# Kernel tuning notes

Measured on AMD Instinct MI355X. Metric: run time of the kernel, lower is better.

Reference implementation:

```python
import jax, jax.numpy as jnp
import numpy as np

K = 2           # top-k experts
TEMP = 1.0      # router temperature


def setup_inputs() -> dict:
    key = jax.random.key(0)
    k0, k1, k2, k3 = jax.random.split(key, 4)
    B, T, C, E = 4, 8192, 1024, 64
    x = jax.random.normal(k0, (B, T, C), dtype=jnp.float32)
    cond = jax.random.normal(k1, (B, C), dtype=jnp.float32)
    # nn.Linear weights: gate (E, C), cond_proj (C, 2C)
    Wg = jax.random.normal(k2, (E, C), dtype=jnp.float32) * 0.02
    Wc = jax.random.normal(k3, (C, 2 * C), dtype=jnp.float32) * 0.02
    return {"x": x, "cond": cond, "Wg": Wg, "Wc": Wc}


def reference(x, cond, Wg, Wc):
    B, T, C = x.shape
    E = Wg.shape[0]
    # conditioning path: broadcast cond over tokens, concat, project
    c_exp = jnp.broadcast_to(cond[:, None, :], (B, T, C))
    hc = jnp.concatenate([x, c_exp], axis=-1)          # (B,T,2C)
    h = jnp.einsum('btd,cd->btc', hc, Wc)              # (B,T,C)
    logits = jnp.einsum('btc,ec->bte', h, Wg) * (1.0 / TEMP)  # (B,T,E)
    probs = jax.nn.softmax(logits, axis=-1)
    topk_vals, idx = jax.lax.top_k(logits, K)          # (B,T,K), sorted desc
    scores = jax.nn.softmax(topk_vals, axis=-1)
    # aux stats (no_grad in torch)
    importance = jax.lax.stop_gradient(jnp.mean(probs, axis=(0, 1)))  # (E,)
    counts = jnp.zeros((E,), probs.dtype).at[idx.reshape(-1)].add(1.0)
    load = counts / jnp.clip(jnp.sum(counts), 1.0)
    load = jax.lax.stop_gradient(load)
    return (idx, scores, probs, importance, load)
```

## Files before the change

### kernel.cpp

```cpp
#include <hip/hip_runtime.h>
#include <math.h>

#define B_    4
#define T_    8192
#define C_    1024
#define E_    64
#define NTOK  (B_*T_)
#define KSEL  2

#define OFF_IDX    0
#define OFF_SCORES (NTOK*KSEL)
#define OFF_PROBS  (2*NTOK*KSEL)
#define OFF_IMP    (OFF_PROBS + NTOK*E_)
#define OFF_LOAD   (OFF_IMP + E_)

#define WS_W64    0
#define WS_W32    1048576
#define WS_BSWH   1310720
#define WS_BSWL   1441792
#define WS_LB64   1572864
#define WS_LB32   1574912
#define WS_CNT    1575936
#define WS_LIST   1576448

#define REFINE_CAP 8192
#define REFINE_EPS 3e-4f

typedef __attribute__((ext_vector_type(8))) short short8;
typedef __attribute__((ext_vector_type(4))) float f32x4;

__global__ __launch_bounds__(256) void k_comb(const float* __restrict__ Wg,
                                              const float* __restrict__ Wc,
                                              double* __restrict__ w64,
                                              float* __restrict__ out,
                                              unsigned int* __restrict__ ref_cnt) {
    __shared__ float wc_s[64 * 64];
    __shared__ float wg_s[64 * 64];
    const int tid   = threadIdx.x;
    const int e     = tid & 63;
    const int dg    = tid >> 6;
    const int dtile = (blockIdx.x & 31) * 64;
    const int cbase = (blockIdx.x >> 5) * 128;

    if (blockIdx.x == 0) {
        if (tid < 2 * E_) out[OFF_IMP + tid] = 0.f;
        if (tid == 2 * E_) *ref_cnt = 0u;
    }

    double acc[16];
#pragma unroll
    for (int i = 0; i < 16; ++i) acc[i] = 0.0;

    for (int cc = 0; cc < 128; cc += 64) {
        const int c0 = cbase + cc;
        __syncthreads();
#pragma unroll
        for (int k = 0; k < 4; ++k) {
            int li = tid + k * 256;
            int r = li >> 4, c4 = (li & 15) * 4;
            *(float4*)&wc_s[r * 64 + c4] =
                *(const float4*)&Wc[(size_t)(c0 + r) * 2048 + dtile + c4];
        }
#pragma unroll
        for (int k = 0; k < 4; ++k) {
            int li = tid + k * 256;
            int r = li >> 4, c4 = (li & 15) * 4;
            float4 v = *(const float4*)&Wg[(size_t)r * 1024 + c0 + c4];
            wg_s[(c4 + 0) * 64 + r] = v.x;
            wg_s[(c4 + 1) * 64 + r] = v.y;
            wg_s[(c4 + 2) * 64 + r] = v.z;
            wg_s[(c4 + 3) * 64 + r] = v.w;
        }
        __syncthreads();
        for (int c = 0; c < 64; ++c) {
            double wg = (double)wg_s[c * 64 + e];
            const float* wcrow = &wc_s[c * 64 + dg * 16];
#pragma unroll
            for (int i = 0; i < 16; ++i)
                acc[i] += wg * (double)wcrow[i];
        }
    }
#pragma unroll
    for (int i = 0; i < 16; ++i) {
        double* p = &w64[(size_t)(dtile + dg * 16 + i) * 64 + e];
#if __has_builtin(__builtin_amdgcn_global_atomic_fadd_f64)
        unsafeAtomicAdd(p, acc[i]);
#else
        atomicAdd(p, acc[i]);
#endif
    }
}

__global__ __launch_bounds__(256) void k_finalize(const double* __restrict__ w64,
                                                  const float* __restrict__ cond,
                                                  float* __restrict__ wcomb32,
                                                  short* __restrict__ bswH,
                                                  short* __restrict__ bswL,
                                                  double* __restrict__ lbias64,
                                                  float* __restrict__ lbias32) {
    const int tid = threadIdx.x;
    if (blockIdx.x < 64) {
        const int e  = blockIdx.x;
        const int et = e >> 4, nn = e & 15;
        for (int d = tid; d < 1024; d += 256) {
            float f = (float)w64[(size_t)d * 64 + e];
            wcomb32[d * 64 + e] = f;
            unsigned u = __float_as_uint(f);
            short hi = (short)(u >> 16);
            float r = f - __uint_as_float(u & 0xFFFF0000u);
            short lo = (short)(__float_as_uint(r) >> 16);
            int kchunk = d >> 5, qsel = (d >> 3) & 3, j = d & 7;
            int idx = ((kchunk * 4 + et) * 64 + qsel * 16 + nn) * 8 + j;
            bswH[idx] = hi;
            bswL[idx] = lo;
        }
    } else {
        const int b = blockIdx.x - 64;
        const int e = tid & 63, part = tid >> 6;
        double acc = 0.0;
        const int d0 = part * 256;
        for (int d = d0; d < d0 + 256; ++d)
            acc += (double)cond[b * 1024 + d] * w64[(size_t)(1024 + d) * 64 + e];
        __shared__ double red[256];
        red[tid] = acc;
        __syncthreads();
        if (tid < 64) {
            double s = red[tid] + red[tid + 64] + red[tid + 128] + red[tid + 192];
            lbias64[b * 64 + tid] = s;
            lbias32[b * 64 + tid] = (float)s;
        }
    }
}

__device__ __forceinline__ void cvt_split8(const float* __restrict__ p,
                                           short8& h, short8& l) {
    float4 v0 = *(const float4*)p;
    float4 v1 = *(const float4*)(p + 4);
    float xv[8] = {v0.x, v0.y, v0.z, v0.w, v1.x, v1.y, v1.z, v1.w};
#pragma unroll
    for (int j = 0; j < 8; ++j) {
        unsigned u = __float_as_uint(xv[j]);
        h[j] = (short)(u >> 16);
        float r = xv[j] - __uint_as_float(u & 0xFFFF0000u);
        l[j] = (short)(__float_as_uint(r) >> 16);
    }
}

#define MT    32
#define ROWP  65

__global__ __launch_bounds__(256, 4) void k_main(const float* __restrict__ x,
                                                 const short* __restrict__ bswH,
                                                 const short* __restrict__ bswL,
                                                 const float* __restrict__ lbias32,
                                                 float* __restrict__ out,
                                                 unsigned int* __restrict__ ref_cnt,
                                                 int* __restrict__ ref_list) {
    __shared__ float accbuf[4 * MT * ROWP];
    __shared__ float invs[MT];
    __shared__ unsigned int cnts[E_];

    const int tid    = threadIdx.x;
    const int wid    = tid >> 6;
    const int lane   = tid & 63;
    const int nn     = lane & 15;
    const int qsel   = lane >> 4;
    const int token0 = blockIdx.x * MT;
    const int b      = token0 >> 13;

    if (tid < E_) cnts[tid] = 0;

    f32x4 acc[2][4];
#pragma unroll
    for (int m = 0; m < 2; ++m)
#pragma unroll
        for (int et = 0; et < 4; ++et) acc[m][et] = (f32x4){0.f, 0.f, 0.f, 0.f};

    const float* a0 = x + (size_t)(token0 + nn) * 1024 + wid * 256 + qsel * 8;
    const float* a1 = a0 + (size_t)16 * 1024;
    const short* bh0 = bswH + ((size_t)(wid * 8) * 4) * 512 + lane * 8;
    const short* bl0 = bswL + ((size_t)(wid * 8) * 4) * 512 + lane * 8;

#pragma unroll 2
    for (int kc = 0; kc < 8; ++kc) {
        short8 ah0, al0, ah1, al1;
        cvt_split8(a0 + kc * 32, ah0, al0);
        cvt_split8(a1 + kc * 32, ah1, al1);
        const short* bh = bh0 + (size_t)kc * 4 * 512;
        const short* bl = bl0 + (size_t)kc * 4 * 512;
#pragma unroll
        for (int et = 0; et < 4; ++et) {
            short8 b_h = *(const short8*)(bh + et * 512);
            short8 b_l = *(const short8*)(bl + et * 512);
            acc[0][et] = __builtin_amdgcn_mfma_f32_16x16x32_bf16(ah0, b_h, acc[0][et], 0, 0, 0);
            acc[0][et] = __builtin_amdgcn_mfma_f32_16x16x32_bf16(ah0, b_l, acc[0][et], 0, 0, 0);
            acc[0][et] = __builtin_amdgcn_mfma_f32_16x16x32_bf16(al0, b_h, acc[0][et], 0, 0, 0);
            acc[1][et] = __builtin_amdgcn_mfma_f32_16x16x32_bf16(ah1, b_h, acc[1][et], 0, 0, 0);
            acc[1][et] = __builtin_amdgcn_mfma_f32_16x16x32_bf16(ah1, b_l, acc[1][et], 0, 0, 0);
            acc[1][et] = __builtin_amdgcn_mfma_f32_16x16x32_bf16(al1, b_h, acc[1][et], 0, 0, 0);
        }
    }

    const int q4 = qsel * 4;
#pragma unroll
    for (int m = 0; m < 2; ++m)
#pragma unroll
        for (int et = 0; et < 4; ++et)
#pragma unroll
            for (int r = 0; r < 4; ++r)
                accbuf[wid * (MT * ROWP) + (m * 16 + q4 + r) * ROWP + et * 16 + nn] =
                    acc[m][et][r];
    __syncthreads();

    for (int li = tid; li < MT * E_; li += 256) {
        int tok = li >> 6, e = li & 63;
        int o = tok * ROWP + e;
        float s = accbuf[o] + accbuf[MT * ROWP + o] + accbuf[2 * MT * ROWP + o] +
                  accbuf[3 * MT * ROWP + o] + lbias32[b * 64 + e];
        accbuf[o] = s;
    }
    __syncthreads();

    if (tid < MT) {
        const int t = tid;
        const int base = t * ROWP;
        float v1 = -1e30f, v2 = -1e30f, v3 = -1e30f;
        int i1 = 0, i2 = 0;
        for (int e = 0; e < E_; ++e) {
            float l = accbuf[base + e];
            if (l > v1)      { v3 = v2; v2 = v1; i2 = i1; v1 = l; i1 = e; }
            else if (l > v2) { v3 = v2; v2 = l; i2 = e; }
            else if (l > v3) { v3 = l; }
        }
        float sum = 0.f;
        for (int e = 0; e < E_; ++e) {
            float ex = __expf(accbuf[base + e] - v1);
            accbuf[base + e] = ex;
            sum += ex;
        }
        invs[t] = 1.0f / sum;

        const int gt = token0 + t;
        float s1 = 1.0f / (1.0f + __expf(v2 - v1));
        *(float2*)&out[OFF_IDX + (size_t)gt * 2]    = make_float2((float)i1, (float)i2);
        *(float2*)&out[OFF_SCORES + (size_t)gt * 2] = make_float2(s1, 1.0f - s1);
        atomicAdd(&cnts[i1], 1u);
        atomicAdd(&cnts[i2], 1u);

        float g12 = v1 - v2, g23 = v2 - v3;
        float g = g12 < g23 ? g12 : g23;
        if (g < REFINE_EPS) {
            unsigned int pos = atomicAdd(ref_cnt, 1u);
            if (pos < REFINE_CAP) ref_list[pos] = gt;
        }
    }
    __syncthreads();

    float* probs = out + OFF_PROBS + (size_t)token0 * E_;
#pragma unroll
    for (int k = 0; k < 2; ++k) {
        int li4 = tid + k * 256;
        int tok = li4 >> 4;
        int c4 = (li4 & 15) << 2;
        float inv = invs[tok];
        int o = tok * ROWP + c4;
        *(float4*)&probs[(size_t)li4 * 4] =
            make_float4(accbuf[o] * inv, accbuf[o + 1] * inv,
                        accbuf[o + 2] * inv, accbuf[o + 3] * inv);
    }

    if (tid < E_) {
        const int e = tid;
        float s = 0.f;
        for (int t = 0; t < MT; ++t) s += accbuf[t * ROWP + e] * invs[t];
        atomicAdd(&out[OFF_IMP + e],  s * (1.0f / (float)NTOK));
        atomicAdd(&out[OFF_LOAD + e], (float)cnts[e] * (1.0f / (float)(NTOK * KSEL)));
    }
}

__global__ __launch_bounds__(256) void k_refine(const float* __restrict__ x,
                                                const float* __restrict__ wcomb32,
                                                const double* __restrict__ lbias64,
                                                const unsigned int* __restrict__ ref_cnt,
                                                const int* __restrict__ ref_list,
                                                float* __restrict__ out) {
    int wave = (int)((blockIdx.x * blockDim.x + threadIdx.x) >> 6);
    int lane = threadIdx.x & 63;
    unsigned int n = *ref_cnt;
    if (n > REFINE_CAP) n = REFINE_CAP;
    const int nwaves = (int)((gridDim.x * blockDim.x) >> 6);

    for (unsigned int wi = wave; wi < n; wi += nwaves) {
        const int gt = ref_list[wi];
        const int b = gt / T_;
        const float* xrow = x + (size_t)gt * C_;
        double a0 = 0.0, a1 = 0.0, a2 = 0.0, a3 = 0.0;
        for (int d = 0; d < C_; d += 4) {
            a0 += (double)xrow[d + 0] * (double)wcomb32[(d + 0) * 64 + lane];
            a1 += (double)xrow[d + 1] * (double)wcomb32[(d + 1) * 64 + lane];
            a2 += (double)xrow[d + 2] * (double)wcomb32[(d + 2) * 64 + lane];
            a3 += (double)xrow[d + 3] * (double)wcomb32[(d + 3) * 64 + lane];
        }
        double acc = ((a0 + a1) + (a2 + a3)) + lbias64[b * 64 + lane];

        double v = acc; int id = lane;
        for (int off = 32; off > 0; off >>= 1) {
            double ov = __shfl_xor(v, off, 64);
            int oid   = __shfl_xor(id, off, 64);
            if (ov > v || (ov == v && oid < id)) { v = ov; id = oid; }
        }
        double v1 = v; int i1 = id;
        v = (lane == i1) ? -1e300 : acc; id = lane;
        for (int off = 32; off > 0; off >>= 1) {
            double ov = __shfl_xor(v, off, 64);
            int oid   = __shfl_xor(id, off, 64);
            if (ov > v || (ov == v && oid < id)) { v = ov; id = oid; }
        }
        double v2 = v; int i2 = id;

        if (lane == 0) {
            float s1 = (float)(1.0 / (1.0 + exp(v2 - v1)));
            *(float2*)&out[OFF_IDX + (size_t)gt * 2]    = make_float2((float)i1, (float)i2);
            *(float2*)&out[OFF_SCORES + (size_t)gt * 2] = make_float2(s1, 1.0f - s1);
        }
    }
}

extern "C" void kernel_launch(void* const* d_in, const int* in_sizes, int n_in,
                              void* d_out, int out_size, void* d_ws, size_t ws_size,
                              hipStream_t stream) {
    const float* x    = (const float*)d_in[0];
    const float* cond = (const float*)d_in[1];
    const float* Wg   = (const float*)d_in[2];
    const float* Wc   = (const float*)d_in[3];
    float* out = (float*)d_out;
    char*  ws  = (char*)d_ws;

    double* w64     = (double*)(ws + WS_W64);
    float*  wcomb32 = (float*)(ws + WS_W32);
    short*  bswH    = (short*)(ws + WS_BSWH);
    short*  bswL    = (short*)(ws + WS_BSWL);
    double* lbias64 = (double*)(ws + WS_LB64);
    float*  lbias32 = (float*)(ws + WS_LB32);
    unsigned int* ref_cnt = (unsigned int*)(ws + WS_CNT);
    int*    ref_list = (int*)(ws + WS_LIST);

    hipMemsetAsync(w64, 0, 2048 * 64 * sizeof(double), stream);

    k_comb<<<256, 256, 0, stream>>>(Wg, Wc, w64, out, ref_cnt);
    k_finalize<<<68, 256, 0, stream>>>(w64, cond, wcomb32, bswH, bswL, lbias64, lbias32);
    k_main<<<NTOK / MT, 256, 0, stream>>>(x, bswH, bswL, lbias32, out, ref_cnt, ref_list);
    k_refine<<<128, 256, 0, stream>>>(x, wcomb32, lbias64, ref_cnt, ref_list, out);
}
```

Measured before the change: 370.0 us.

## Halve main-kernel token tile, raise occupancy, use nontemporal x loads, widen finalize grid

The main kernel now handles 16 tokens per block instead of 32, so it uses half the accumulators and LDS and can declare 8 waves-per-SIMD occupancy with twice as many blocks. Loads of x go through nontemporal builtins so the streamed activations do not pollute the cache. The finalize kernel spreads the weight-conversion work over 256 blocks instead of 64. The trade-off is that each block reloads the same B fragments for fewer tokens, which doubles B-weight traffic per token and adds per-block fixed costs such as the atomics on importance and load.

```diff
diff --git a/kernel.cpp b/kernel.cpp
--- a/kernel.cpp
+++ b/kernel.cpp
@@ -99,23 +99,23 @@
                                                   double* __restrict__ lbias64,
                                                   float* __restrict__ lbias32) {
     const int tid = threadIdx.x;
-    if (blockIdx.x < 64) {
-        const int e  = blockIdx.x;
+    if (blockIdx.x < 256) {
+        const int e  = blockIdx.x & 63;
+        const int dq = blockIdx.x >> 6;
         const int et = e >> 4, nn = e & 15;
-        for (int d = tid; d < 1024; d += 256) {
-            float f = (float)w64[(size_t)d * 64 + e];
-            wcomb32[d * 64 + e] = f;
-            unsigned u = __float_as_uint(f);
-            short hi = (short)(u >> 16);
-            float r = f - __uint_as_float(u & 0xFFFF0000u);
-            short lo = (short)(__float_as_uint(r) >> 16);
-            int kchunk = d >> 5, qsel = (d >> 3) & 3, j = d & 7;
-            int idx = ((kchunk * 4 + et) * 64 + qsel * 16 + nn) * 8 + j;
-            bswH[idx] = hi;
-            bswL[idx] = lo;
-        }
+        const int d  = dq * 256 + tid;
+        float f = (float)w64[(size_t)d * 64 + e];
+        wcomb32[d * 64 + e] = f;
+        unsigned u = __float_as_uint(f);
+        short hi = (short)(u >> 16);
+        float r = f - __uint_as_float(u & 0xFFFF0000u);
+        short lo = (short)(__float_as_uint(r) >> 16);
+        int kchunk = d >> 5, qsel = (d >> 3) & 3, j = d & 7;
+        int idx = ((kchunk * 4 + et) * 64 + qsel * 16 + nn) * 8 + j;
+        bswH[idx] = hi;
+        bswL[idx] = lo;
     } else {
-        const int b = blockIdx.x - 64;
+        const int b = blockIdx.x - 256;
         const int e = tid & 63, part = tid >> 6;
         double acc = 0.0;
         const int d0 = part * 256;
@@ -132,11 +132,11 @@
     }
 }
 
-__device__ __forceinline__ void cvt_split8(const float* __restrict__ p,
-                                           short8& h, short8& l) {
-    float4 v0 = *(const float4*)p;
-    float4 v1 = *(const float4*)(p + 4);
-    float xv[8] = {v0.x, v0.y, v0.z, v0.w, v1.x, v1.y, v1.z, v1.w};
+__device__ __forceinline__ void cvt_split8_nt(const float* __restrict__ p,
+                                              short8& h, short8& l) {
+    f32x4 v0 = __builtin_nontemporal_load((const f32x4*)p);
+    f32x4 v1 = __builtin_nontemporal_load(((const f32x4*)p) + 1);
+    float xv[8] = {v0[0], v0[1], v0[2], v0[3], v1[0], v1[1], v1[2], v1[3]};
 #pragma unroll
     for (int j = 0; j < 8; ++j) {
         unsigned u = __float_as_uint(xv[j]);
@@ -146,10 +146,10 @@
     }
 }
 
-#define MT    32
+#define MT    16
 #define ROWP  65
 
-__global__ __launch_bounds__(256, 4) void k_main(const float* __restrict__ x,
+__global__ __launch_bounds__(256, 8) void k_main(const float* __restrict__ x,
                                                  const short* __restrict__ bswH,
                                                  const short* __restrict__ bswL,
                                                  const float* __restrict__ lbias32,
@@ -170,46 +170,36 @@
 
     if (tid < E_) cnts[tid] = 0;
 
-    f32x4 acc[2][4];
-#pragma unroll
-    for (int m = 0; m < 2; ++m)
-#pragma unroll
-        for (int et = 0; et < 4; ++et) acc[m][et] = (f32x4){0.f, 0.f, 0.f, 0.f};
+    f32x4 acc[4];
+#pragma unroll
+    for (int et = 0; et < 4; ++et) acc[et] = (f32x4){0.f, 0.f, 0.f, 0.f};
 
     const float* a0 = x + (size_t)(token0 + nn) * 1024 + wid * 256 + qsel * 8;
-    const float* a1 = a0 + (size_t)16 * 1024;
     const short* bh0 = bswH + ((size_t)(wid * 8) * 4) * 512 + lane * 8;
     const short* bl0 = bswL + ((size_t)(wid * 8) * 4) * 512 + lane * 8;
 
 #pragma unroll 2
     for (int kc = 0; kc < 8; ++kc) {
-        short8 ah0, al0, ah1, al1;
-        cvt_split8(a0 + kc * 32, ah0, al0);
-        cvt_split8(a1 + kc * 32, ah1, al1);
+        short8 ah, al;
+        cvt_split8_nt(a0 + kc * 32, ah, al);
         const short* bh = bh0 + (size_t)kc * 4 * 512;
         const short* bl = bl0 + (size_t)kc * 4 * 512;
 #pragma unroll
         for (int et = 0; et < 4; ++et) {
             short8 b_h = *(const short8*)(bh + et * 512);
             short8 b_l = *(const short8*)(bl + et * 512);
-            acc[0][et] = __builtin_amdgcn_mfma_f32_16x16x32_bf16(ah0, b_h, acc[0][et], 0, 0, 0);
-            acc[0][et] = __builtin_amdgcn_mfma_f32_16x16x32_bf16(ah0, b_l, acc[0][et], 0, 0, 0);
-            acc[0][et] = __builtin_amdgcn_mfma_f32_16x16x32_bf16(al0, b_h, acc[0][et], 0, 0, 0);
-            acc[1][et] = __builtin_amdgcn_mfma_f32_16x16x32_bf16(ah1, b_h, acc[1][et], 0, 0, 0);
-            acc[1][et] = __builtin_amdgcn_mfma_f32_16x16x32_bf16(ah1, b_l, acc[1][et], 0, 0, 0);
-            acc[1][et] = __builtin_amdgcn_mfma_f32_16x16x32_bf16(al1, b_h, acc[1][et], 0, 0, 0);
+            acc[et] = __builtin_amdgcn_mfma_f32_16x16x32_bf16(ah, b_h, acc[et], 0, 0, 0);
+            acc[et] = __builtin_amdgcn_mfma_f32_16x16x32_bf16(ah, b_l, acc[et], 0, 0, 0);
+            acc[et] = __builtin_amdgcn_mfma_f32_16x16x32_bf16(al, b_h, acc[et], 0, 0, 0);
         }
     }
 
     const int q4 = qsel * 4;
 #pragma unroll
-    for (int m = 0; m < 2; ++m)
-#pragma unroll
-        for (int et = 0; et < 4; ++et)
-#pragma unroll
-            for (int r = 0; r < 4; ++r)
-                accbuf[wid * (MT * ROWP) + (m * 16 + q4 + r) * ROWP + et * 16 + nn] =
-                    acc[m][et][r];
+    for (int et = 0; et < 4; ++et)
+#pragma unroll
+        for (int r = 0; r < 4; ++r)
+            accbuf[wid * (MT * ROWP) + (q4 + r) * ROWP + et * 16 + nn] = acc[et][r];
     __syncthreads();
 
     for (int li = tid; li < MT * E_; li += 256) {
@@ -256,15 +246,13 @@
     }
     __syncthreads();
 
-    float* probs = out + OFF_PROBS + (size_t)token0 * E_;
-#pragma unroll
-    for (int k = 0; k < 2; ++k) {
-        int li4 = tid + k * 256;
-        int tok = li4 >> 4;
-        int c4 = (li4 & 15) << 2;
+    {
+        float* probs = out + OFF_PROBS + (size_t)token0 * E_;
+        int tok = tid >> 4;
+        int c4 = (tid & 15) << 2;
         float inv = invs[tok];
         int o = tok * ROWP + c4;
-        *(float4*)&probs[(size_t)li4 * 4] =
+        *(float4*)&probs[(size_t)tid * 4] =
             make_float4(accbuf[o] * inv, accbuf[o + 1] * inv,
                         accbuf[o + 2] * inv, accbuf[o + 3] * inv);
     }
@@ -348,7 +336,7 @@
     hipMemsetAsync(w64, 0, 2048 * 64 * sizeof(double), stream);
 
     k_comb<<<256, 256, 0, stream>>>(Wg, Wc, w64, out, ref_cnt);
-    k_finalize<<<68, 256, 0, stream>>>(w64, cond, wcomb32, bswH, bswL, lbias64, lbias32);
+    k_finalize<<<260, 256, 0, stream>>>(w64, cond, wcomb32, bswH, bswL, lbias64, lbias32);
     k_main<<<NTOK / MT, 256, 0, stream>>>(x, bswH, bswL, lbias32, out, ref_cnt, ref_list);
     k_refine<<<128, 256, 0, stream>>>(x, wcomb32, lbias64, ref_cnt, ref_list, out);
 }
```

Measured after the change: 405.0 us. 9.5% more time.
